# Kernel tuning notes

Measured on AMD Instinct MI355X. Metric: run time of the kernel, lower is better.

## Reference

```python
import jax, jax.numpy as jnp
import numpy as np

BATCH, SEQ, IN_DIM = 512, 512, 64
H1, H2, OUT = 100, 100, 1


def setup_inputs() -> dict:
    key = jax.random.key(0)
    ks = jax.random.split(key, 7)
    s = lambda fan_in: 1.0 / np.sqrt(fan_in)
    return {
        "x":   jax.random.normal(ks[0], (BATCH, SEQ, IN_DIM), dtype=jnp.float32),
        "W1x": jax.random.normal(ks[1], (IN_DIM, H1), dtype=jnp.float32) * s(IN_DIM),
        "W1h": jax.random.normal(ks[2], (H1, H1), dtype=jnp.float32) * s(H1),
        "b1":  jnp.zeros((H1,), dtype=jnp.float32),
        "W2x": jax.random.normal(ks[3], (H1, H2), dtype=jnp.float32) * s(H1),
        "W2h": jax.random.normal(ks[4], (H2, H2), dtype=jnp.float32) * s(H2),
        "b2":  jnp.zeros((H2,), dtype=jnp.float32),
        "Wo":  jax.random.normal(ks[5], (H2, OUT), dtype=jnp.float32) * s(H2),
        "bo":  jnp.zeros((OUT,), dtype=jnp.float32),
    }


def reference(x, W1x, W1h, b1, W2x, W2h, b2, Wo, bo):
    # Two stacked SimpleRNN layers (tanh), fused in a single scan over time.
    # Keras SimpleRNN: h_t = tanh(x_t @ Wx + h_{t-1} @ Wh + b)
    B = x.shape[0]
    h1_0 = jnp.zeros((B, W1h.shape[0]), dtype=x.dtype)
    h2_0 = jnp.zeros((B, W2h.shape[0]), dtype=x.dtype)

    def step(carry, x_t):
        h1, h2 = carry
        h1 = jnp.tanh(x_t @ W1x + h1 @ W1h + b1)   # [B, H1]
        h2 = jnp.tanh(h1 @ W2x + h2 @ W2h + b2)    # [B, H2]
        return (h1, h2), None

    xs = jnp.swapaxes(x, 0, 1)                      # [T, B, D]
    (h1_T, h2_T), _ = jax.lax.scan(step, (h1_0, h2_0), xs)
    out = h2_T @ Wo + bo                            # [B, 1]
    return out, h1_T, h2_T
```

## Files before the change

kernel.cpp:

```cpp
#include <hip/hip_runtime.h>
#include <math.h>

#define T      512
#define NBATCH 512
#define IN_DIM 64
#define H      100
#define KP     208
#define PBYTES 832

__device__ __forceinline__ float fast_tanh(float a) {
    float e = __expf(2.0f * a);
    return 1.0f - 2.0f / (e + 1.0f);
}

#define DPP_ADD(v, ctrl) ((v) + __int_as_float(__builtin_amdgcn_update_dpp( \
        0, __float_as_int(v), (ctrl), 0xF, 0xF, true)))
#define RED8(a) { (a) = DPP_ADD((a), 0xB1);    \
                  (a) = DPP_ADD((a), 0x4E);    \
                  (a) = DPP_ADD((a), 0x128);   }

__device__ __forceinline__ float wval(const float* __restrict__ WA,
                                      const float* __restrict__ WB,
                                      int kA, int R, int col) {
    if (R < kA) return WA[R * H + col];
    int rr = R - kA;
    return (rr < H) ? WB[rr * H + col] : 0.f;
}

__device__ __forceinline__ float4 wload4(const float* __restrict__ WA,
                                         const float* __restrict__ WB,
                                         int kA, int R0, int col) {
    return make_float4(wval(WA, WB, kA, R0 + 0, col),
                       wval(WA, WB, kA, R0 + 1, col),
                       wval(WA, WB, kA, R0 + 2, col),
                       wval(WA, WB, kA, R0 + 3, col));
}


#define RNDS(X) X(0) X(1) X(2) X(3) X(4) X(5)

#define WDECL(R) float4 w##R##_0 = {0,0,0,0}, w##R##_1 = {0,0,0,0}, \
                        w##R##_2 = {0,0,0,0}, w##R##_3 = {0,0,0,0};

#define WLOAD(R) { const int r0_ = 32 * (R) + 4 * s;   \
    w##R##_0 = wload4(WA, WB, kA, r0_, j + 0);         \
    w##R##_1 = wload4(WA, WB, kA, r0_, j + 1);         \
    w##R##_2 = wload4(WA, WB, kA, r0_, j + 2);         \
    w##R##_3 = wload4(WA, WB, kA, r0_, j + 3); }

#define FSTEP(R, P) { const float4 v_ = *(const float4*)(rb + (P) + 128 * (R)); \
    a0 = fmaf(v_.x, w##R##_0.x, a0); a1 = fmaf(v_.x, w##R##_1.x, a1);           \
    a2 = fmaf(v_.x, w##R##_2.x, a2); a3 = fmaf(v_.x, w##R##_3.x, a3);           \
    a0 = fmaf(v_.y, w##R##_0.y, a0); a1 = fmaf(v_.y, w##R##_1.y, a1);           \
    a2 = fmaf(v_.y, w##R##_2.y, a2); a3 = fmaf(v_.y, w##R##_3.y, a3);           \
    a0 = fmaf(v_.z, w##R##_0.z, a0); a1 = fmaf(v_.z, w##R##_1.z, a1);           \
    a2 = fmaf(v_.z, w##R##_2.z, a2); a3 = fmaf(v_.z, w##R##_3.z, a3);           \
    a0 = fmaf(v_.w, w##R##_0.w, a0); a1 = fmaf(v_.w, w##R##_1.w, a1);           \
    a2 = fmaf(v_.w, w##R##_2.w, a2); a3 = fmaf(v_.w, w##R##_3.w, a3); }

#define DOT(P, hv) {                                                 \
    float a0 = 0.f, a1 = 0.f, a2 = 0.f, a3 = 0.f;                    \
    FSTEP(0, P) FSTEP(1, P) FSTEP(2, P)                              \
    FSTEP(3, P) FSTEP(4, P) FSTEP(5, P)                              \
    { const float2 v_ = *(const float2*)(tb + (P));                  \
      a0 = fmaf(v_.x, wt0.x, a0); a1 = fmaf(v_.x, wt1.x, a1);        \
      a2 = fmaf(v_.x, wt2.x, a2); a3 = fmaf(v_.x, wt3.x, a3);        \
      a0 = fmaf(v_.y, wt0.y, a0); a1 = fmaf(v_.y, wt1.y, a1);        \
      a2 = fmaf(v_.y, wt2.y, a2); a3 = fmaf(v_.y, wt3.y, a3); }      \
    RED8(a0) RED8(a1) RED8(a2) RED8(a3)                              \
    const float t01_ = (s & 1) ? a1 : a0;                            \
    const float t23_ = (s & 1) ? a3 : a2;                            \
    hv = fast_tanh(((s & 2) ? t23_ : t01_) + bj); }

__global__ __launch_bounds__(512, 4)
void drnn_kernel(const float* __restrict__ x,
                 const float* __restrict__ W1x, const float* __restrict__ W1h,
                 const float* __restrict__ b1,
                 const float* __restrict__ W2x, const float* __restrict__ W2h,
                 const float* __restrict__ b2,
                 const float* __restrict__ Wo,  const float* __restrict__ bo,
                 float* __restrict__ out)
{
    __shared__ __align__(16) float in1[2][KP];
    __shared__ __align__(16) float in2[2][KP];

    const int tid  = threadIdx.x;
    const int b    = blockIdx.x;
    const int lane = tid & 63;
    const int wv   = tid >> 6;
    const int s    = (lane & 3) | ((lane >> 1) & 4);
    const int gw   = ((lane >> 2) & 1) | ((lane >> 3) & 6);
    const int gg   = wv * 8 + gw;
    const bool active = (gg < 50);
    const bool isL1   = (gg < 25);
    const bool isXL   = (wv == 7);

    const float* __restrict__ xrow = x + (size_t)b * T * IN_DIM;

    for (int k = tid; k < 2 * KP; k += 512) {
        (&in1[0][0])[k] = 0.f;
        (&in2[0][0])[k] = 0.f;
    }
    if (tid < IN_DIM) in1[0][tid] = xrow[tid];

    const float* __restrict__ WA = isL1 ? W1x : W2x;
    const float* __restrict__ WB = isL1 ? W1h : W2h;
    const int kA = isL1 ? IN_DIM : H;
    const int gl = isL1 ? gg : gg - 25;
    const int nl = (gl >= 0 && gl < 25) ? gl : 0;
    const int j  = 4 * nl;
    const int n  = j + (s & 3);
    const float bj = active ? (isL1 ? b1 : b2)[n] : 0.f;

    RNDS(WDECL)
    float2 wt0 = {0,0}, wt1 = {0,0}, wt2 = {0,0}, wt3 = {0,0};
    if (active) {
        RNDS(WLOAD)
        const int rt = 192 + 2 * s;
        wt0 = make_float2(wval(WA,WB,kA,rt,j+0), wval(WA,WB,kA,rt+1,j+0));
        wt1 = make_float2(wval(WA,WB,kA,rt,j+1), wval(WA,WB,kA,rt+1,j+1));
        wt2 = make_float2(wval(WA,WB,kA,rt,j+2), wval(WA,WB,kA,rt+1,j+2));
        wt3 = make_float2(wval(WA,WB,kA,rt,j+3), wval(WA,WB,kA,rt+1,j+3));
    }

    const char* lb = (const char*)(isL1 ? &in1[0][0] : &in2[0][0]);
    const char* rb = lb + 16 * s;
    const char* tb = lb + 768 + 8 * s;

    char* st;
    if (isL1) st = (char*)((s < 4) ? &in1[0][64 + n] : &in2[0][n]);
    else      st = (char*)&in2[0][100 + n];
    const bool dost = active && (isL1 || s < 4);

    char* xw = (char*)&in1[0][lane];
    float xr0 = 0.f, xr1 = 0.f;
    if (isXL) {
        xr0 = xrow[IN_DIM + lane];
        xr1 = xrow[2 * IN_DIM + lane];
    }

    __syncthreads();

    #pragma unroll 1
    for (int i = 0; i < T; i += 2) {
        if (active) {
            float hv; DOT(0, hv)
            if (dost && (isL1 || i > 0)) *(float*)(st + PBYTES) = hv;
        } else if (isXL) {
            *(float*)(xw + PBYTES) = xr0;
            xr0 = xr1;
            if (i + 3 < T) xr1 = xrow[(size_t)(i + 3) * IN_DIM + lane];
        }
        __syncthreads();
        if (active) {
            float hv; DOT(PBYTES, hv)
            if (dost) *(float*)st = hv;
        } else if (isXL) {
            *(float*)xw = xr0;
            xr0 = xr1;
            if (i + 4 < T) xr1 = xrow[(size_t)(i + 4) * IN_DIM + lane];
        }
        __syncthreads();
    }

    if (active && !isL1) {
        float hv; DOT(0, hv)
        if (s < 4) *(float*)(st + PBYTES) = hv;
    }
    __syncthreads();

    if (tid < H)
        out[NBATCH + (size_t)b * H + tid] = in1[0][64 + tid];
    if (tid < H)
        out[NBATCH + (size_t)NBATCH * H + (size_t)b * H + tid] = in2[1][100 + tid];

    if (tid < 64) {
        float v = in2[1][100 + tid] * Wo[tid];
        if (tid + 64 < H) v += in2[1][100 + 64 + tid] * Wo[tid + 64];
        #pragma unroll
        for (int off = 32; off >= 1; off >>= 1) v += __shfl_down(v, off);
        if (tid == 0) out[b] = v + bo[0];
    }
}

extern "C" void kernel_launch(void* const* d_in, const int* in_sizes, int n_in,
                              void* d_out, int out_size, void* d_ws, size_t ws_size,
                              hipStream_t stream) {
    const float* x   = (const float*)d_in[0];
    const float* W1x = (const float*)d_in[1];
    const float* W1h = (const float*)d_in[2];
    const float* b1  = (const float*)d_in[3];
    const float* W2x = (const float*)d_in[4];
    const float* W2h = (const float*)d_in[5];
    const float* b2  = (const float*)d_in[6];
    const float* Wo  = (const float*)d_in[7];
    const float* bo  = (const float*)d_in[8];
    float* out = (float*)d_out;

    drnn_kernel<<<NBATCH, 512, 0, stream>>>(x, W1x, W1h, b1, W2x, W2h, b2,
                                            Wo, bo, out);
}
```

Baseline: 512.4 us.

## Repartition matvec into 16-lane units with packed FP32 FMA and transpose-style DPP reduction

Reorganizes the per-step recurrent matvec so each 16-lane group computes 8 output columns (instead of 8-lane groups computing 4), using v_pk_fma_f32 inline asm to do two FMAs per instruction over paired rows. The cross-lane reduction becomes a butterfly that halves the number of live partial sums at each DPP stage instead of reducing four accumulators independently. The intent is to cut VALU instruction count on the serial critical path of each timestep. It adds padding columns clamped to H-1 with masked stores, conditional tail handling for some waves, and a #define of b1 that shadows a kernel parameter name.

```diff
diff --git a/kernel.cpp b/kernel.cpp
--- a/kernel.cpp
+++ b/kernel.cpp
@@ -8,69 +8,80 @@
 #define KP     208
 #define PBYTES 832
 
+typedef float f2 __attribute__((ext_vector_type(2)));
+
 __device__ __forceinline__ float fast_tanh(float a) {
     float e = __expf(2.0f * a);
     return 1.0f - 2.0f / (e + 1.0f);
 }
 
-#define DPP_ADD(v, ctrl) ((v) + __int_as_float(__builtin_amdgcn_update_dpp( \
-        0, __float_as_int(v), (ctrl), 0xF, 0xF, true)))
-#define RED8(a) { (a) = DPP_ADD((a), 0xB1);    \
-                  (a) = DPP_ADD((a), 0x4E);    \
-                  (a) = DPP_ADD((a), 0x128);   }
-
-__device__ __forceinline__ float wval(const float* __restrict__ WA,
-                                      const float* __restrict__ WB,
-                                      int kA, int R, int col) {
-    if (R < kA) return WA[R * H + col];
-    int rr = R - kA;
-    return (rr < H) ? WB[rr * H + col] : 0.f;
-}
-
-__device__ __forceinline__ float4 wload4(const float* __restrict__ WA,
-                                         const float* __restrict__ WB,
-                                         int kA, int R0, int col) {
-    return make_float4(wval(WA, WB, kA, R0 + 0, col),
-                       wval(WA, WB, kA, R0 + 1, col),
-                       wval(WA, WB, kA, R0 + 2, col),
-                       wval(WA, WB, kA, R0 + 3, col));
-}
-
-
-#define RNDS(X) X(0) X(1) X(2) X(3) X(4) X(5)
-
-#define WDECL(R) float4 w##R##_0 = {0,0,0,0}, w##R##_1 = {0,0,0,0}, \
-                        w##R##_2 = {0,0,0,0}, w##R##_3 = {0,0,0,0};
-
-#define WLOAD(R) { const int r0_ = 32 * (R) + 4 * s;   \
-    w##R##_0 = wload4(WA, WB, kA, r0_, j + 0);         \
-    w##R##_1 = wload4(WA, WB, kA, r0_, j + 1);         \
-    w##R##_2 = wload4(WA, WB, kA, r0_, j + 2);         \
-    w##R##_3 = wload4(WA, WB, kA, r0_, j + 3); }
-
-#define FSTEP(R, P) { const float4 v_ = *(const float4*)(rb + (P) + 128 * (R)); \
-    a0 = fmaf(v_.x, w##R##_0.x, a0); a1 = fmaf(v_.x, w##R##_1.x, a1);           \
-    a2 = fmaf(v_.x, w##R##_2.x, a2); a3 = fmaf(v_.x, w##R##_3.x, a3);           \
-    a0 = fmaf(v_.y, w##R##_0.y, a0); a1 = fmaf(v_.y, w##R##_1.y, a1);           \
-    a2 = fmaf(v_.y, w##R##_2.y, a2); a3 = fmaf(v_.y, w##R##_3.y, a3);           \
-    a0 = fmaf(v_.z, w##R##_0.z, a0); a1 = fmaf(v_.z, w##R##_1.z, a1);           \
-    a2 = fmaf(v_.z, w##R##_2.z, a2); a3 = fmaf(v_.z, w##R##_3.z, a3);           \
-    a0 = fmaf(v_.w, w##R##_0.w, a0); a1 = fmaf(v_.w, w##R##_1.w, a1);           \
-    a2 = fmaf(v_.w, w##R##_2.w, a2); a3 = fmaf(v_.w, w##R##_3.w, a3); }
-
-#define DOT(P, hv) {                                                 \
-    float a0 = 0.f, a1 = 0.f, a2 = 0.f, a3 = 0.f;                    \
-    FSTEP(0, P) FSTEP(1, P) FSTEP(2, P)                              \
-    FSTEP(3, P) FSTEP(4, P) FSTEP(5, P)                              \
-    { const float2 v_ = *(const float2*)(tb + (P));                  \
-      a0 = fmaf(v_.x, wt0.x, a0); a1 = fmaf(v_.x, wt1.x, a1);        \
-      a2 = fmaf(v_.x, wt2.x, a2); a3 = fmaf(v_.x, wt3.x, a3);        \
-      a0 = fmaf(v_.y, wt0.y, a0); a1 = fmaf(v_.y, wt1.y, a1);        \
-      a2 = fmaf(v_.y, wt2.y, a2); a3 = fmaf(v_.y, wt3.y, a3); }      \
-    RED8(a0) RED8(a1) RED8(a2) RED8(a3)                              \
-    const float t01_ = (s & 1) ? a1 : a0;                            \
-    const float t23_ = (s & 1) ? a3 : a2;                            \
-    hv = fast_tanh(((s & 2) ? t23_ : t01_) + bj); }
+#define PKFMA_LO(acc, va, w) \
+    asm("v_pk_fma_f32 %0, %1, %2, %0 op_sel:[0,0,0] op_sel_hi:[0,1,1]" \
+        : "+v"(acc) : "v"(va), "v"(w));
+#define PKFMA_HI(acc, va, w) \
+    asm("v_pk_fma_f32 %0, %1, %2, %0 op_sel:[1,0,0] op_sel_hi:[1,1,1]" \
+        : "+v"(acc) : "v"(va), "v"(w));
+
+#define DPPMOV(x, ctrl) __int_as_float(__builtin_amdgcn_update_dpp( \
+        0, __float_as_int(x), (ctrl), 0xF, 0xF, true))
+
+__device__ __forceinline__ f2 wload2(const float* __restrict__ WA,
+                                     const float* __restrict__ WB,
+                                     int kA, int R, int ca, int cb) {
+    f2 r;
+    if (R < kA)             { r.x = WA[R * H + ca];  r.y = WA[R * H + cb]; }
+    else {
+        int rr = R - kA;
+        if (rr < H)         { r.x = WB[rr * H + ca]; r.y = WB[rr * H + cb]; }
+        else                { r.x = 0.f;             r.y = 0.f; }
+    }
+    return r;
+}
+
+
+#define WRDECL(r) f2 w##r##a_0={0,0}, w##r##a_1={0,0}, w##r##a_2={0,0}, w##r##a_3={0,0}, \
+                     w##r##b_0={0,0}, w##r##b_1={0,0}, w##r##b_2={0,0}, w##r##b_3={0,0};
+
+#define WRLOAD(r) { const int Ra_ = 32 * (r) + 2 * s, Rb_ = Ra_ + 1;      \
+    w##r##a_0 = wload2(WA, WB, kA, Ra_, c0, c1);                          \
+    w##r##a_1 = wload2(WA, WB, kA, Ra_, c2, c3);                          \
+    w##r##a_2 = wload2(WA, WB, kA, Ra_, c4, c5);                          \
+    w##r##a_3 = wload2(WA, WB, kA, Ra_, c6, c7);                          \
+    w##r##b_0 = wload2(WA, WB, kA, Rb_, c0, c1);                          \
+    w##r##b_1 = wload2(WA, WB, kA, Rb_, c2, c3);                          \
+    w##r##b_2 = wload2(WA, WB, kA, Rb_, c4, c5);                          \
+    w##r##b_3 = wload2(WA, WB, kA, Rb_, c6, c7); }
+
+#define ROUND(r, P) { const f2 va_ = *(const f2*)(rb + (P) + 128 * (r));  \
+    PKFMA_LO(A0, va_, w##r##a_0) PKFMA_LO(A1, va_, w##r##a_1)             \
+    PKFMA_LO(A2, va_, w##r##a_2) PKFMA_LO(A3, va_, w##r##a_3)             \
+    PKFMA_HI(A0, va_, w##r##b_0) PKFMA_HI(A1, va_, w##r##b_1)             \
+    PKFMA_HI(A2, va_, w##r##b_2) PKFMA_HI(A3, va_, w##r##b_3) }
+
+#define DOT(P, hv) {                                                      \
+    f2 A0={0,0}, A1={0,0}, A2={0,0}, A3={0,0};                            \
+    ROUND(0, P) ROUND(1, P) ROUND(2, P)                                   \
+    ROUND(3, P) ROUND(4, P) ROUND(5, P)                                   \
+    if (hasTail) {                                                        \
+        const float vt_ = *(const float*)(tb + (P));                      \
+        A0.x = fmaf(vt_, wt_0.x, A0.x); A0.y = fmaf(vt_, wt_0.y, A0.y);   \
+        A1.x = fmaf(vt_, wt_1.x, A1.x); A1.y = fmaf(vt_, wt_1.y, A1.y);   \
+        A2.x = fmaf(vt_, wt_2.x, A2.x); A2.y = fmaf(vt_, wt_2.y, A2.y);   \
+        A3.x = fmaf(vt_, wt_3.x, A3.x); A3.y = fmaf(vt_, wt_3.y, A3.y);   \
+    }                                                                     \
+             \
+    float u0_ = (b0 ? A0.y : A0.x) + DPPMOV(b0 ? A0.x : A0.y, 0xB1);      \
+    float u1_ = (b0 ? A1.y : A1.x) + DPPMOV(b0 ? A1.x : A1.y, 0xB1);      \
+    float u2_ = (b0 ? A2.y : A2.x) + DPPMOV(b0 ? A2.x : A2.y, 0xB1);      \
+    float u3_ = (b0 ? A3.y : A3.x) + DPPMOV(b0 ? A3.x : A3.y, 0xB1);      \
+                         \
+    float v0_ = (b1 ? u1_ : u0_) + DPPMOV(b1 ? u0_ : u1_, 0x4E);          \
+    float v1_ = (b1 ? u3_ : u2_) + DPPMOV(b1 ? u2_ : u3_, 0x4E);          \
+             \
+    float z_  = (b3 ? v1_ : v0_) + DPPMOV(b3 ? v0_ : v1_, 0x128);         \
+     \
+    z_ += DPPMOV(DPPMOV(z_, 0x141), 0x1B);                                \
+    hv = fast_tanh(z_ + bj); }
 
 __global__ __launch_bounds__(512, 4)
 void drnn_kernel(const float* __restrict__ x,
@@ -88,12 +99,12 @@
     const int b    = blockIdx.x;
     const int lane = tid & 63;
     const int wv   = tid >> 6;
-    const int s    = (lane & 3) | ((lane >> 1) & 4);
-    const int gw   = ((lane >> 2) & 1) | ((lane >> 3) & 6);
-    const int gg   = wv * 8 + gw;
-    const bool active = (gg < 50);
-    const bool isL1   = (gg < 25);
+    const int s    = lane & 15;
+    const int unit = wv * 4 + (lane >> 4);
+    const bool active = (unit < 26);
+    const bool isL1   = (unit < 13);
     const bool isXL   = (wv == 7);
+    const bool hasTail = (wv >= 3);
 
     const float* __restrict__ xrow = x + (size_t)b * T * IN_DIM;
 
@@ -106,31 +117,39 @@
     const float* __restrict__ WA = isL1 ? W1x : W2x;
     const float* __restrict__ WB = isL1 ? W1h : W2h;
     const int kA = isL1 ? IN_DIM : H;
-    const int gl = isL1 ? gg : gg - 25;
-    const int nl = (gl >= 0 && gl < 25) ? gl : 0;
-    const int j  = 4 * nl;
-    const int n  = j + (s & 3);
-    const float bj = active ? (isL1 ? b1 : b2)[n] : 0.f;
-
-    RNDS(WDECL)
-    float2 wt0 = {0,0}, wt1 = {0,0}, wt2 = {0,0}, wt3 = {0,0};
+    const int ul = isL1 ? unit : unit - 13;
+    const int j  = 8 * ((ul >= 0 && ul < 13) ? ul : 0);
+    const int colof = (lane & 3) | ((lane >> 1) & 4);
+    const int n  = j + colof;
+    const bool dost = active && (n < H);
+    const int nc = (n < H) ? n : H - 1;
+    const float bj = active ? (isL1 ? b1 : b2)[nc] : 0.f;
+    const int c0 = (j+0<H)?j+0:H-1, c1 = (j+1<H)?j+1:H-1, c2 = (j+2<H)?j+2:H-1, c3 = (j+3<H)?j+3:H-1;
+    const int c4 = (j+4<H)?j+4:H-1, c5 = (j+5<H)?j+5:H-1, c6 = (j+6<H)?j+6:H-1, c7 = (j+7<H)?j+7:H-1;
+
+    const bool b0 = (lane & 1) != 0;
+    const bool b1_ = (lane & 2) != 0;
+    const bool b3 = (lane & 8) != 0;
+    #define b1 b1_
+
+    WRDECL(0) WRDECL(1) WRDECL(2) WRDECL(3) WRDECL(4) WRDECL(5)
+    f2 wt_0={0,0}, wt_1={0,0}, wt_2={0,0}, wt_3={0,0};
     if (active) {
-        RNDS(WLOAD)
-        const int rt = 192 + 2 * s;
-        wt0 = make_float2(wval(WA,WB,kA,rt,j+0), wval(WA,WB,kA,rt+1,j+0));
-        wt1 = make_float2(wval(WA,WB,kA,rt,j+1), wval(WA,WB,kA,rt+1,j+1));
-        wt2 = make_float2(wval(WA,WB,kA,rt,j+2), wval(WA,WB,kA,rt+1,j+2));
-        wt3 = make_float2(wval(WA,WB,kA,rt,j+3), wval(WA,WB,kA,rt+1,j+3));
+        WRLOAD(0) WRLOAD(1) WRLOAD(2) WRLOAD(3) WRLOAD(4) WRLOAD(5)
+        const int Rt = 192 + s;
+        wt_0 = wload2(WA, WB, kA, Rt, c0, c1);
+        wt_1 = wload2(WA, WB, kA, Rt, c2, c3);
+        wt_2 = wload2(WA, WB, kA, Rt, c4, c5);
+        wt_3 = wload2(WA, WB, kA, Rt, c6, c7);
     }
 
     const char* lb = (const char*)(isL1 ? &in1[0][0] : &in2[0][0]);
-    const char* rb = lb + 16 * s;
-    const char* tb = lb + 768 + 8 * s;
+    const char* rb = lb + 8 * s;
+    const char* tb = lb + 768 + 4 * s;
 
     char* st;
-    if (isL1) st = (char*)((s < 4) ? &in1[0][64 + n] : &in2[0][n]);
+    if (isL1) st = (char*)((lane & 4) ? &in2[0][n] : &in1[0][64 + n]);
     else      st = (char*)&in2[0][100 + n];
-    const bool dost = active && (isL1 || s < 4);
 
     char* xw = (char*)&in1[0][lane];
     float xr0 = 0.f, xr1 = 0.f;
@@ -165,7 +184,7 @@
 
     if (active && !isL1) {
         float hv; DOT(0, hv)
-        if (s < 4) *(float*)(st + PBYTES) = hv;
+        if (dost) *(float*)(st + PBYTES) = hv;
     }
     __syncthreads();
 
@@ -181,6 +200,7 @@
         for (int off = 32; off >= 1; off >>= 1) v += __shfl_down(v, off);
         if (tid == 0) out[b] = v + bo[0];
     }
+    #undef b1
 }
 
 extern "C" void kernel_launch(void* const* d_in, const int* in_sizes, int n_in,
```

Result: slower. 570.2 us (+11.3%).

## Restructure RNN dot into 16-lane units with transpose-reduce and precomputed x projection

Applied to the files above, without the earlier changes.

Each group of 16 lanes now computes 8 output columns, and the cross-lane sum uses a transpose-style DPP reduction so no lanes duplicate work. Layer 1's input projection x_t·W1x is computed one step ahead, off the critical path, from a new shared ring buffer for x, so the recurrent dot per step only covers the hidden part. Layer 2 folds its tail row into a scalar seed. This is meant to cut FMAs and DPP ops per step on the serial time loop. The cost is more registers (eight accumulators and 24 float4 weights) and extra ring-buffer bookkeeping.

```diff
diff --git a/kernel.cpp b/kernel.cpp
--- a/kernel.cpp
+++ b/kernel.cpp
@@ -13,11 +13,8 @@
     return 1.0f - 2.0f / (e + 1.0f);
 }
 
-#define DPP_ADD(v, ctrl) ((v) + __int_as_float(__builtin_amdgcn_update_dpp( \
-        0, __float_as_int(v), (ctrl), 0xF, 0xF, true)))
-#define RED8(a) { (a) = DPP_ADD((a), 0xB1);    \
-                  (a) = DPP_ADD((a), 0x4E);    \
-                  (a) = DPP_ADD((a), 0x128);   }
+#define DPPMOV(x, ctrl) __int_as_float(__builtin_amdgcn_update_dpp( \
+        0, __float_as_int(x), (ctrl), 0xF, 0xF, true))
 
 __device__ __forceinline__ float wval(const float* __restrict__ WA,
                                       const float* __restrict__ WB,
@@ -37,40 +34,52 @@
 }
 
 
-#define RNDS(X) X(0) X(1) X(2) X(3) X(4) X(5)
-
-#define WDECL(R) float4 w##R##_0 = {0,0,0,0}, w##R##_1 = {0,0,0,0}, \
-                        w##R##_2 = {0,0,0,0}, w##R##_3 = {0,0,0,0};
-
-#define WLOAD(R) { const int r0_ = 32 * (R) + 4 * s;   \
-    w##R##_0 = wload4(WA, WB, kA, r0_, j + 0);         \
-    w##R##_1 = wload4(WA, WB, kA, r0_, j + 1);         \
-    w##R##_2 = wload4(WA, WB, kA, r0_, j + 2);         \
-    w##R##_3 = wload4(WA, WB, kA, r0_, j + 3); }
-
-#define FSTEP(R, P) { const float4 v_ = *(const float4*)(rb + (P) + 128 * (R)); \
-    a0 = fmaf(v_.x, w##R##_0.x, a0); a1 = fmaf(v_.x, w##R##_1.x, a1);           \
-    a2 = fmaf(v_.x, w##R##_2.x, a2); a3 = fmaf(v_.x, w##R##_3.x, a3);           \
-    a0 = fmaf(v_.y, w##R##_0.y, a0); a1 = fmaf(v_.y, w##R##_1.y, a1);           \
-    a2 = fmaf(v_.y, w##R##_2.y, a2); a3 = fmaf(v_.y, w##R##_3.y, a3);           \
-    a0 = fmaf(v_.z, w##R##_0.z, a0); a1 = fmaf(v_.z, w##R##_1.z, a1);           \
-    a2 = fmaf(v_.z, w##R##_2.z, a2); a3 = fmaf(v_.z, w##R##_3.z, a3);           \
-    a0 = fmaf(v_.w, w##R##_0.w, a0); a1 = fmaf(v_.w, w##R##_1.w, a1);           \
-    a2 = fmaf(v_.w, w##R##_2.w, a2); a3 = fmaf(v_.w, w##R##_3.w, a3); }
-
-#define DOT(P, hv) {                                                 \
-    float a0 = 0.f, a1 = 0.f, a2 = 0.f, a3 = 0.f;                    \
-    FSTEP(0, P) FSTEP(1, P) FSTEP(2, P)                              \
-    FSTEP(3, P) FSTEP(4, P) FSTEP(5, P)                              \
-    { const float2 v_ = *(const float2*)(tb + (P));                  \
-      a0 = fmaf(v_.x, wt0.x, a0); a1 = fmaf(v_.x, wt1.x, a1);        \
-      a2 = fmaf(v_.x, wt2.x, a2); a3 = fmaf(v_.x, wt3.x, a3);        \
-      a0 = fmaf(v_.y, wt0.y, a0); a1 = fmaf(v_.y, wt1.y, a1);        \
-      a2 = fmaf(v_.y, wt2.y, a2); a3 = fmaf(v_.y, wt3.y, a3); }      \
-    RED8(a0) RED8(a1) RED8(a2) RED8(a3)                              \
-    const float t01_ = (s & 1) ? a1 : a0;                            \
-    const float t23_ = (s & 1) ? a3 : a2;                            \
-    hv = fast_tanh(((s & 2) ? t23_ : t01_) + bj); }
+#define FMA4(r, c, v) { a##c = fmaf((v).x, w##r##_##c.x, a##c); \
+                        a##c = fmaf((v).y, w##r##_##c.y, a##c); \
+                        a##c = fmaf((v).z, w##r##_##c.z, a##c); \
+                        a##c = fmaf((v).w, w##r##_##c.w, a##c); }
+#define FROUND(r, v) FMA4(r,0,v) FMA4(r,1,v) FMA4(r,2,v) FMA4(r,3,v) \
+                     FMA4(r,4,v) FMA4(r,5,v) FMA4(r,6,v) FMA4(r,7,v)
+
+#define WDECL(c) float4 w0_##c = {0,0,0,0}, w1_##c = {0,0,0,0}, w2_##c = {0,0,0,0};
+#define WLOADC(c) { w0_##c = wload4(WA, WB, kA,       4*s, cc##c); \
+                    w1_##c = wload4(WA, WB, kA,  64 + 4*s, cc##c); \
+                    w2_##c = wload4(WA, WB, kA, 128 + 4*s, cc##c); }
+#define WCOLS(X) X(0) X(1) X(2) X(3) X(4) X(5) X(6) X(7)
+
+#define SH1(c) { p##c = xv_.x * w0_##c.x; p##c = fmaf(xv_.y, w0_##c.y, p##c); \
+                 p##c = fmaf(xv_.z, w0_##c.z, p##c); p##c = fmaf(xv_.w, w0_##c.w, p##c); }
+#define SHCOLS() SH1(0) SH1(1) SH1(2) SH1(3) SH1(4) SH1(5) SH1(6) SH1(7)
+
+#define SHADOW() { const float4 xv_ = *(const float4*)xptr; SHCOLS() \
+    xptr += 256; if (xptr >= xend) xptr -= 768; }
+
+#define XLOAD(wr_t, ld_t) { if ((wr_t) < T) *(float*)xptr = p0; p0 = p1;   \
+    if ((ld_t) < T) p1 = xrow[(size_t)(ld_t) * IN_DIM + lane];             \
+    xptr += 256; if (xptr >= xend) xptr -= 768; }
+
+#define DOTCORE(P, hv) {                                                   \
+    float a0,a1,a2,a3,a4,a5,a6,a7;                                         \
+    const float4 v1_ = *(const float4*)(rb + (P) + 256);                   \
+    const float4 v2_ = *(const float4*)(rb + (P) + 512);                   \
+    if (isL1) { a0=p0; a1=p1; a2=p2; a3=p3; a4=p4; a5=p5; a6=p6; a7=p7; }  \
+    else {                                                                 \
+        const float4 v0_ = *(const float4*)(rb + (P));                     \
+        const float  vt_ = *(const float*)(tb + (P));                      \
+        a0 = vt_*p0; a1 = vt_*p1; a2 = vt_*p2; a3 = vt_*p3;                \
+        a4 = vt_*p4; a5 = vt_*p5; a6 = vt_*p6; a7 = vt_*p7;                \
+        FROUND(0, v0_)                                                     \
+    }                                                                      \
+    FROUND(1, v1_) FROUND(2, v2_)                                          \
+    float u0_ = (q0 ? a1 : a0) + DPPMOV(q0 ? a0 : a1, 0xB1);               \
+    float u1_ = (q0 ? a3 : a2) + DPPMOV(q0 ? a2 : a3, 0xB1);               \
+    float u2_ = (q0 ? a5 : a4) + DPPMOV(q0 ? a4 : a5, 0xB1);               \
+    float u3_ = (q0 ? a7 : a6) + DPPMOV(q0 ? a6 : a7, 0xB1);               \
+    float r0_ = (q1 ? u1_ : u0_) + DPPMOV(q1 ? u0_ : u1_, 0x4E);           \
+    float r1_ = (q1 ? u3_ : u2_) + DPPMOV(q1 ? u2_ : u3_, 0x4E);           \
+    float z_  = (q3 ? r1_ : r0_) + DPPMOV(q3 ? r0_ : r1_, 0x128);          \
+    z_ += DPPMOV(DPPMOV(z_, 0x141), 0x1B);                                 \
+    hv = fast_tanh(z_ + bj); }
 
 __global__ __launch_bounds__(512, 4)
 void drnn_kernel(const float* __restrict__ x,
@@ -83,16 +92,16 @@
 {
     __shared__ __align__(16) float in1[2][KP];
     __shared__ __align__(16) float in2[2][KP];
+    __shared__ __align__(16) float xring[3][IN_DIM];
 
     const int tid  = threadIdx.x;
     const int b    = blockIdx.x;
     const int lane = tid & 63;
     const int wv   = tid >> 6;
-    const int s    = (lane & 3) | ((lane >> 1) & 4);
-    const int gw   = ((lane >> 2) & 1) | ((lane >> 3) & 6);
-    const int gg   = wv * 8 + gw;
-    const bool active = (gg < 50);
-    const bool isL1   = (gg < 25);
+    const int s    = lane & 15;
+    const int unit = wv * 4 + (lane >> 4);
+    const bool active = (unit < 26);
+    const bool isL1   = (unit < 13);
     const bool isXL   = (wv == 7);
 
     const float* __restrict__ xrow = x + (size_t)b * T * IN_DIM;
@@ -101,71 +110,82 @@
         (&in1[0][0])[k] = 0.f;
         (&in2[0][0])[k] = 0.f;
     }
-    if (tid < IN_DIM) in1[0][tid] = xrow[tid];
 
     const float* __restrict__ WA = isL1 ? W1x : W2x;
     const float* __restrict__ WB = isL1 ? W1h : W2h;
     const int kA = isL1 ? IN_DIM : H;
-    const int gl = isL1 ? gg : gg - 25;
-    const int nl = (gl >= 0 && gl < 25) ? gl : 0;
-    const int j  = 4 * nl;
-    const int n  = j + (s & 3);
-    const float bj = active ? (isL1 ? b1 : b2)[n] : 0.f;
-
-    RNDS(WDECL)
-    float2 wt0 = {0,0}, wt1 = {0,0}, wt2 = {0,0}, wt3 = {0,0};
+    const int ul = isL1 ? unit : unit - 13;
+    const int j  = 8 * ((ul >= 0 && ul < 13) ? ul : 0);
+    const int colof = (lane & 3) | ((lane >> 1) & 4);
+    const int n  = j + colof;
+    const int nc = (n < H) ? n : H - 1;
+    const float bj = active ? (isL1 ? b1 : b2)[nc] : 0.f;
+    const int cc0=(j+0<H)?j+0:H-1, cc1=(j+1<H)?j+1:H-1, cc2=(j+2<H)?j+2:H-1, cc3=(j+3<H)?j+3:H-1;
+    const int cc4=(j+4<H)?j+4:H-1, cc5=(j+5<H)?j+5:H-1, cc6=(j+6<H)?j+6:H-1, cc7=(j+7<H)?j+7:H-1;
+
+    const bool q0 = (lane & 1) != 0;
+    const bool q1 = (lane & 2) != 0;
+    const bool q3 = (lane & 8) != 0;
+
+    WCOLS(WDECL)
+    float p0=0.f,p1=0.f,p2=0.f,p3=0.f,p4=0.f,p5=0.f,p6=0.f,p7=0.f;
     if (active) {
-        RNDS(WLOAD)
-        const int rt = 192 + 2 * s;
-        wt0 = make_float2(wval(WA,WB,kA,rt,j+0), wval(WA,WB,kA,rt+1,j+0));
-        wt1 = make_float2(wval(WA,WB,kA,rt,j+1), wval(WA,WB,kA,rt+1,j+1));
-        wt2 = make_float2(wval(WA,WB,kA,rt,j+2), wval(WA,WB,kA,rt+1,j+2));
-        wt3 = make_float2(wval(WA,WB,kA,rt,j+3), wval(WA,WB,kA,rt+1,j+3));
-    }
-
-    const char* lb = (const char*)(isL1 ? &in1[0][0] : &in2[0][0]);
-    const char* rb = lb + 16 * s;
-    const char* tb = lb + 768 + 8 * s;
-
-    char* st;
-    if (isL1) st = (char*)((s < 4) ? &in1[0][64 + n] : &in2[0][n]);
-    else      st = (char*)&in2[0][100 + n];
-    const bool dost = active && (isL1 || s < 4);
-
-    char* xw = (char*)&in1[0][lane];
-    float xr0 = 0.f, xr1 = 0.f;
+        WCOLS(WLOADC)
+        if (!isL1) {
+            const int Rt = 192 + s;
+            p0 = wval(WA,WB,kA,Rt,cc0); p1 = wval(WA,WB,kA,Rt,cc1);
+            p2 = wval(WA,WB,kA,Rt,cc2); p3 = wval(WA,WB,kA,Rt,cc3);
+            p4 = wval(WA,WB,kA,Rt,cc4); p5 = wval(WA,WB,kA,Rt,cc5);
+            p6 = wval(WA,WB,kA,Rt,cc6); p7 = wval(WA,WB,kA,Rt,cc7);
+        }
+    }
+
+    const char* rb = (const char*)(isL1 ? &in1[0][0] : &in2[0][0]) + 16 * s;
+    const char* tb = (const char*)&in2[0][0] + 768 + 4 * s;
+
+    char* st; bool dow;
+    if (isL1) { st = (char*)((lane & 4) ? &in2[0][n] : &in1[0][64 + n]);
+                dow = active && (n < H); }
+    else      { st = (char*)&in2[0][100 + n];
+                dow = active && (n < H) && !(lane & 4); }
+
+    const int  xoff = isXL ? 4 * lane : 16 * s;
+    char*       xptr = (char*)&xring[0][0] + (isXL ? 512 : 256) + xoff;
+    const char* xend = (char*)&xring[0][0] + 768 + xoff;
+
     if (isXL) {
-        xr0 = xrow[IN_DIM + lane];
-        xr1 = xrow[2 * IN_DIM + lane];
+        xring[0][lane] = xrow[lane];
+        xring[1][lane] = xrow[IN_DIM + lane];
+        p0 = xrow[2 * IN_DIM + lane];
+        p1 = xrow[3 * IN_DIM + lane];
     }
 
     __syncthreads();
+
+    if (active && isL1) {
+        const float4 xv_ = *(const float4*)((const char*)&xring[0][0] + 16 * s);
+        SHCOLS()
+    }
 
     #pragma unroll 1
     for (int i = 0; i < T; i += 2) {
         if (active) {
-            float hv; DOT(0, hv)
-            if (dost && (isL1 || i > 0)) *(float*)(st + PBYTES) = hv;
-        } else if (isXL) {
-            *(float*)(xw + PBYTES) = xr0;
-            xr0 = xr1;
-            if (i + 3 < T) xr1 = xrow[(size_t)(i + 3) * IN_DIM + lane];
-        }
+            float hv; DOTCORE(0, hv)
+            if (dow && (isL1 || i > 0)) *(float*)(st + PBYTES) = hv;
+            if (isL1) SHADOW()
+        } else if (isXL) { XLOAD(i + 2, i + 4) }
         __syncthreads();
         if (active) {
-            float hv; DOT(PBYTES, hv)
-            if (dost) *(float*)st = hv;
-        } else if (isXL) {
-            *(float*)xw = xr0;
-            xr0 = xr1;
-            if (i + 4 < T) xr1 = xrow[(size_t)(i + 4) * IN_DIM + lane];
-        }
+            float hv; DOTCORE(PBYTES, hv)
+            if (dow) *(float*)st = hv;
+            if (isL1) SHADOW()
+        } else if (isXL) { XLOAD(i + 3, i + 5) }
         __syncthreads();
     }
 
     if (active && !isL1) {
-        float hv; DOT(0, hv)
-        if (s < 4) *(float*)(st + PBYTES) = hv;
+        float hv; DOTCORE(0, hv)
+        if (dow) *(float*)(st + PBYTES) = hv;
     }
     __syncthreads();
 
```

Measured after the change: 753.5 us. 1.47x slower.

## Repartition RNN dot products into 16-lane units with 16 outputs each

Applied to the files above, without the earlier changes.

Work is repartitioned so each 16-lane group computes 16 output columns over a 208-long input vector, with weights held in registers and partial sums combined by a transpose-style DPP butterfly reduction. This halves the block to 256 threads and reduces the number of idle lanes. The x-streaming work is split between two spare units that load float4 chunks on alternating half-steps. In exchange, register pressure per thread rises (about 208 weight floats), which may limit occupancy. The reduction tree also becomes more intricate.

```diff
diff --git a/kernel.cpp b/kernel.cpp
--- a/kernel.cpp
+++ b/kernel.cpp
@@ -13,66 +13,74 @@
     return 1.0f - 2.0f / (e + 1.0f);
 }
 
-#define DPP_ADD(v, ctrl) ((v) + __int_as_float(__builtin_amdgcn_update_dpp( \
-        0, __float_as_int(v), (ctrl), 0xF, 0xF, true)))
-#define RED8(a) { (a) = DPP_ADD((a), 0xB1);    \
-                  (a) = DPP_ADD((a), 0x4E);    \
-                  (a) = DPP_ADD((a), 0x128);   }
-
-__device__ __forceinline__ float wval(const float* __restrict__ WA,
-                                      const float* __restrict__ WB,
-                                      int kA, int R, int col) {
+#define DPPMOV(x, ctrl) __int_as_float(__builtin_amdgcn_update_dpp( \
+        0, __float_as_int(x), (ctrl), 0xF, 0xF, true))
+
+__device__ __forceinline__ float wvalc(const float* __restrict__ WA,
+                                       const float* __restrict__ WB,
+                                       int kA, int R, int col) {
+    if (col >= H) return 0.f;
     if (R < kA) return WA[R * H + col];
     int rr = R - kA;
     return (rr < H) ? WB[rr * H + col] : 0.f;
 }
 
-__device__ __forceinline__ float4 wload4(const float* __restrict__ WA,
-                                         const float* __restrict__ WB,
-                                         int kA, int R0, int col) {
-    return make_float4(wval(WA, WB, kA, R0 + 0, col),
-                       wval(WA, WB, kA, R0 + 1, col),
-                       wval(WA, WB, kA, R0 + 2, col),
-                       wval(WA, WB, kA, R0 + 3, col));
-}
-
-
-#define RNDS(X) X(0) X(1) X(2) X(3) X(4) X(5)
-
-#define WDECL(R) float4 w##R##_0 = {0,0,0,0}, w##R##_1 = {0,0,0,0}, \
-                        w##R##_2 = {0,0,0,0}, w##R##_3 = {0,0,0,0};
-
-#define WLOAD(R) { const int r0_ = 32 * (R) + 4 * s;   \
-    w##R##_0 = wload4(WA, WB, kA, r0_, j + 0);         \
-    w##R##_1 = wload4(WA, WB, kA, r0_, j + 1);         \
-    w##R##_2 = wload4(WA, WB, kA, r0_, j + 2);         \
-    w##R##_3 = wload4(WA, WB, kA, r0_, j + 3); }
-
-#define FSTEP(R, P) { const float4 v_ = *(const float4*)(rb + (P) + 128 * (R)); \
-    a0 = fmaf(v_.x, w##R##_0.x, a0); a1 = fmaf(v_.x, w##R##_1.x, a1);           \
-    a2 = fmaf(v_.x, w##R##_2.x, a2); a3 = fmaf(v_.x, w##R##_3.x, a3);           \
-    a0 = fmaf(v_.y, w##R##_0.y, a0); a1 = fmaf(v_.y, w##R##_1.y, a1);           \
-    a2 = fmaf(v_.y, w##R##_2.y, a2); a3 = fmaf(v_.y, w##R##_3.y, a3);           \
-    a0 = fmaf(v_.z, w##R##_0.z, a0); a1 = fmaf(v_.z, w##R##_1.z, a1);           \
-    a2 = fmaf(v_.z, w##R##_2.z, a2); a3 = fmaf(v_.z, w##R##_3.z, a3);           \
-    a0 = fmaf(v_.w, w##R##_0.w, a0); a1 = fmaf(v_.w, w##R##_1.w, a1);           \
-    a2 = fmaf(v_.w, w##R##_2.w, a2); a3 = fmaf(v_.w, w##R##_3.w, a3); }
-
-#define DOT(P, hv) {                                                 \
-    float a0 = 0.f, a1 = 0.f, a2 = 0.f, a3 = 0.f;                    \
-    FSTEP(0, P) FSTEP(1, P) FSTEP(2, P)                              \
-    FSTEP(3, P) FSTEP(4, P) FSTEP(5, P)                              \
-    { const float2 v_ = *(const float2*)(tb + (P));                  \
-      a0 = fmaf(v_.x, wt0.x, a0); a1 = fmaf(v_.x, wt1.x, a1);        \
-      a2 = fmaf(v_.x, wt2.x, a2); a3 = fmaf(v_.x, wt3.x, a3);        \
-      a0 = fmaf(v_.y, wt0.y, a0); a1 = fmaf(v_.y, wt1.y, a1);        \
-      a2 = fmaf(v_.y, wt2.y, a2); a3 = fmaf(v_.y, wt3.y, a3); }      \
-    RED8(a0) RED8(a1) RED8(a2) RED8(a3)                              \
-    const float t01_ = (s & 1) ? a1 : a0;                            \
-    const float t23_ = (s & 1) ? a3 : a2;                            \
-    hv = fast_tanh(((s & 2) ? t23_ : t01_) + bj); }
-
-__global__ __launch_bounds__(512, 4)
+__device__ __forceinline__ float4 wload4c(const float* __restrict__ WA,
+                                          const float* __restrict__ WB,
+                                          int kA, int R0, int col) {
+    return make_float4(wvalc(WA, WB, kA, R0 + 0, col),
+                       wvalc(WA, WB, kA, R0 + 1, col),
+                       wvalc(WA, WB, kA, R0 + 2, col),
+                       wvalc(WA, WB, kA, R0 + 3, col));
+}
+
+
+#define K16(X) X(0) X(1) X(2) X(3) X(4) X(5) X(6) X(7) \
+               X(8) X(9) X(10) X(11) X(12) X(13) X(14) X(15)
+
+#define WDECL(k) float4 w0_##k={0,0,0,0}, w1_##k={0,0,0,0}, w2_##k={0,0,0,0}; \
+                 float wt##k = 0.f;
+#define WLOAD(k) { const int ck_ = j + ((k) ^ cl);                \
+    w0_##k = wload4c(WA, WB, kA,        4*l, ck_);                \
+    w1_##k = wload4c(WA, WB, kA,  64 + 4*l, ck_);                 \
+    w2_##k = wload4c(WA, WB, kA, 128 + 4*l, ck_);                 \
+    wt##k  = wvalc (WA, WB, kA, 192 + l,   ck_); }
+
+#define ADECL(k) float a##k = 0.f;
+#define FR0(k) { a##k = fmaf(v0_.x, w0_##k.x, a##k); a##k = fmaf(v0_.y, w0_##k.y, a##k); \
+                 a##k = fmaf(v0_.z, w0_##k.z, a##k); a##k = fmaf(v0_.w, w0_##k.w, a##k); }
+#define FR1(k) { a##k = fmaf(v1_.x, w1_##k.x, a##k); a##k = fmaf(v1_.y, w1_##k.y, a##k); \
+                 a##k = fmaf(v1_.z, w1_##k.z, a##k); a##k = fmaf(v1_.w, w1_##k.w, a##k); }
+#define FR2(k) { a##k = fmaf(v2_.x, w2_##k.x, a##k); a##k = fmaf(v2_.y, w2_##k.y, a##k); \
+                 a##k = fmaf(v2_.z, w2_##k.z, a##k); a##k = fmaf(v2_.w, w2_##k.w, a##k); }
+#define FT(k)  { a##k = fmaf(vt_, wt##k, a##k); }
+
+#define DOTCORE(P, hv) {                                                  \
+    const float4 v0_ = *(const float4*)(rb + (P));                        \
+    const float4 v1_ = *(const float4*)(rb + (P) + 256);                  \
+    const float4 v2_ = *(const float4*)(rb + (P) + 512);                  \
+    const float  vt_ = *(const float*)(tb + (P));                         \
+    K16(ADECL)                                                            \
+    K16(FR0) K16(FR1) K16(FR2)                                            \
+    if (hasTail) { K16(FT) }                                              \
+    float u0_ = a0  + DPPMOV(a1,  0xB1);                                  \
+    float u1_ = a2  + DPPMOV(a3,  0xB1);                                  \
+    float u2_ = a4  + DPPMOV(a5,  0xB1);                                  \
+    float u3_ = a6  + DPPMOV(a7,  0xB1);                                  \
+    float u4_ = a8  + DPPMOV(a9,  0xB1);                                  \
+    float u5_ = a10 + DPPMOV(a11, 0xB1);                                  \
+    float u6_ = a12 + DPPMOV(a13, 0xB1);                                  \
+    float u7_ = a14 + DPPMOV(a15, 0xB1);                                  \
+    float r0_ = u0_ + DPPMOV(u1_, 0x4E);                                  \
+    float r1_ = u2_ + DPPMOV(u3_, 0x4E);                                  \
+    float r2_ = u4_ + DPPMOV(u5_, 0x4E);                                  \
+    float r3_ = u6_ + DPPMOV(u7_, 0x4E);                                  \
+    float z0_ = r0_ + DPPMOV(r1_, 0x128);                                 \
+    float z1_ = r2_ + DPPMOV(r3_, 0x128);                                 \
+    float zz_ = z0_ + DPPMOV(DPPMOV(z1_, 0x141), 0x1B);                   \
+    hv = fast_tanh(zz_ + bj); }
+
+__global__ __launch_bounds__(256, 2)
 void drnn_kernel(const float* __restrict__ x,
                  const float* __restrict__ W1x, const float* __restrict__ W1h,
                  const float* __restrict__ b1,
@@ -86,18 +94,18 @@
 
     const int tid  = threadIdx.x;
     const int b    = blockIdx.x;
-    const int lane = tid & 63;
     const int wv   = tid >> 6;
-    const int s    = (lane & 3) | ((lane >> 1) & 4);
-    const int gw   = ((lane >> 2) & 1) | ((lane >> 3) & 6);
-    const int gg   = wv * 8 + gw;
-    const bool active = (gg < 50);
-    const bool isL1   = (gg < 25);
-    const bool isXL   = (wv == 7);
+    const int l    = tid & 15;
+    const int unit = tid >> 4;
+    const bool comp  = (unit < 14);
+    const bool isL1  = (unit < 7);
+    const bool isX14 = (unit == 14);
+    const bool isX15 = (unit == 15);
+    const bool hasTail = (wv >= 1);
 
     const float* __restrict__ xrow = x + (size_t)b * T * IN_DIM;
 
-    for (int k = tid; k < 2 * KP; k += 512) {
+    for (int k = tid; k < 2 * KP; k += 256) {
         (&in1[0][0])[k] = 0.f;
         (&in2[0][0])[k] = 0.f;
     }
@@ -106,66 +114,65 @@
     const float* __restrict__ WA = isL1 ? W1x : W2x;
     const float* __restrict__ WB = isL1 ? W1h : W2h;
     const int kA = isL1 ? IN_DIM : H;
-    const int gl = isL1 ? gg : gg - 25;
-    const int nl = (gl >= 0 && gl < 25) ? gl : 0;
-    const int j  = 4 * nl;
-    const int n  = j + (s & 3);
-    const float bj = active ? (isL1 ? b1 : b2)[n] : 0.f;
-
-    RNDS(WDECL)
-    float2 wt0 = {0,0}, wt1 = {0,0}, wt2 = {0,0}, wt3 = {0,0};
-    if (active) {
-        RNDS(WLOAD)
-        const int rt = 192 + 2 * s;
-        wt0 = make_float2(wval(WA,WB,kA,rt,j+0), wval(WA,WB,kA,rt+1,j+0));
-        wt1 = make_float2(wval(WA,WB,kA,rt,j+1), wval(WA,WB,kA,rt+1,j+1));
-        wt2 = make_float2(wval(WA,WB,kA,rt,j+2), wval(WA,WB,kA,rt+1,j+2));
-        wt3 = make_float2(wval(WA,WB,kA,rt,j+3), wval(WA,WB,kA,rt+1,j+3));
-    }
+    const int ul = isL1 ? unit : unit - 7;
+    const int j  = 16 * ((ul < 7) ? ul : 0);
+    const int cl = (l & 3) | ((l >> 1) & 4) | ((l & 4) << 1);
+    const int n  = j + cl;
+    const bool stok = (n < H);
+    const int nc = stok ? n : H - 1;
+    const float bj = comp ? (isL1 ? b1 : b2)[nc] : 0.f;
+
+    K16(WDECL)
+    if (comp) { K16(WLOAD) }
 
     const char* lb = (const char*)(isL1 ? &in1[0][0] : &in2[0][0]);
-    const char* rb = lb + 16 * s;
-    const char* tb = lb + 768 + 8 * s;
-
-    char* st;
-    if (isL1) st = (char*)((s < 4) ? &in1[0][64 + n] : &in2[0][n]);
-    else      st = (char*)&in2[0][100 + n];
-    const bool dost = active && (isL1 || s < 4);
-
-    char* xw = (char*)&in1[0][lane];
-    float xr0 = 0.f, xr1 = 0.f;
-    if (isXL) {
-        xr0 = xrow[IN_DIM + lane];
-        xr1 = xrow[2 * IN_DIM + lane];
-    }
+    const char* rb = lb + 16 * l;
+    const char* tb = lb + 768 + 4 * l;
+
+    char* stA = (char*)&in1[0][64 + nc];
+    char* stB = (char*)&in2[0][nc];
+    char* stC = (char*)&in2[0][100 + nc];
+
+    float4 xr = {0.f, 0.f, 0.f, 0.f};
+    if (isX14) xr = *(const float4*)(xrow + 1 * IN_DIM + 4 * l);
+    if (isX15) xr = *(const float4*)(xrow + 2 * IN_DIM + 4 * l);
+    char* xw14 = (char*)&in1[1][4 * l];
+    char* xw15 = (char*)&in1[0][4 * l];
 
     __syncthreads();
 
     #pragma unroll 1
     for (int i = 0; i < T; i += 2) {
-        if (active) {
-            float hv; DOT(0, hv)
-            if (dost && (isL1 || i > 0)) *(float*)(st + PBYTES) = hv;
-        } else if (isXL) {
-            *(float*)(xw + PBYTES) = xr0;
-            xr0 = xr1;
-            if (i + 3 < T) xr1 = xrow[(size_t)(i + 3) * IN_DIM + lane];
+        if (comp) {
+            float hv; DOTCORE(0, hv)
+            if (isL1) {
+                if (stok) { *(float*)(stA + PBYTES) = hv;
+                            *(float*)(stB + PBYTES) = hv; }
+            } else if (stok && i > 0) {
+                *(float*)(stC + PBYTES) = hv;
+            }
+        } else if (isX14) {
+            *(float4*)xw14 = xr;
+            if (i + 3 < T) xr = *(const float4*)(xrow + (size_t)(i + 3) * IN_DIM + 4 * l);
         }
         __syncthreads();
-        if (active) {
-            float hv; DOT(PBYTES, hv)
-            if (dost) *(float*)st = hv;
-        } else if (isXL) {
-            *(float*)xw = xr0;
-            xr0 = xr1;
-            if (i + 4 < T) xr1 = xrow[(size_t)(i + 4) * IN_DIM + lane];
+        if (comp) {
+            float hv; DOTCORE(PBYTES, hv)
+            if (isL1) {
+                if (stok) { *(float*)stA = hv; *(float*)stB = hv; }
+            } else if (stok) {
+                *(float*)stC = hv;
+            }
+        } else if (isX15) {
+            *(float4*)xw15 = xr;
+            if (i + 4 < T) xr = *(const float4*)(xrow + (size_t)(i + 4) * IN_DIM + 4 * l);
         }
         __syncthreads();
     }
 
-    if (active && !isL1) {
-        float hv; DOT(0, hv)
-        if (s < 4) *(float*)(st + PBYTES) = hv;
+    if (comp && !isL1) {
+        float hv; DOTCORE(0, hv)
+        if (stok) *(float*)(stC + PBYTES) = hv;
     }
     __syncthreads();
 
@@ -197,6 +204,6 @@
     const float* bo  = (const float*)d_in[8];
     float* out = (float*)d_out;
 
-    drnn_kernel<<<NBATCH, 512, 0, stream>>>(x, W1x, W1h, b1, W2x, W2h, b2,
+    drnn_kernel<<<NBATCH, 256, 0, stream>>>(x, W1x, W1h, b1, W2x, W2h, b2,
                                             Wo, bo, out);
 }
```

Measured after the change: 621.1 us. 1.21x slower.
